# Kernel tuning notes

Hardware: AMD Instinct MI355X
Metric: run time of the kernel (lower is better)

The kernel has to match this reference:

```python
import jax, jax.numpy as jnp
import numpy as np

BN_EPS = 1e-5

def _deg_inv_sqrt(idx, n):
    deg = jax.ops.segment_sum(jnp.ones(idx.shape, jnp.float32), idx, num_segments=n)
    return jnp.where(deg > 0, 1.0 / jnp.sqrt(jnp.maximum(deg, 1.0)), 0.0)

def setup_inputs() -> dict:
    key = jax.random.key(0)
    ks = jax.random.split(key, 8)
    N, E, D, L = 50000, 500000, 128, 3
    node_ids = jax.random.randint(ks[0], (N,), 0, 343)
    src = jax.random.randint(ks[1], (E,), 0, N, dtype=jnp.int32)
    dst = jax.random.randint(ks[2], (E,), 0, N, dtype=jnp.int32)
    emb_table = jax.random.normal(ks[3], (343, D), jnp.float32)
    s = 1.0 / np.sqrt(D)
    Ws = jax.random.normal(ks[4], (L, D, D), jnp.float32) * s
    bs = jnp.zeros((L, D), jnp.float32)
    Rws = jax.random.normal(ks[5], (L, D, D), jnp.float32) * s
    Rbs = jnp.zeros((L, D), jnp.float32)
    gammas = jnp.ones((L, D), jnp.float32)
    betas = jnp.zeros((L, D), jnp.float32)
    return dict(node_ids=node_ids, src=src, dst=dst, emb_table=emb_table,
                Ws=Ws, bs=bs, Rws=Rws, Rbs=Rbs, gammas=gammas, betas=betas)

def reference(node_ids, src, dst, emb_table, Ws, bs, Rws, Rbs, gammas, betas):
    N = node_ids.shape[0]
    L = Ws.shape[0]
    # GraphConv norm='both': src side uses out-degree, dst side uses in-degree
    out_norm = _deg_inv_sqrt(src, N)  # [N]
    in_norm = _deg_inv_sqrt(dst, N)   # [N]
    x = emb_table[node_ids]           # [N, D] embedding lookup
    for l in range(L):
        # D^{-1/2} A D^{-1/2} X, then linear + bias + activation (DGL GraphConv)
        h = x * out_norm[:, None]
        agg = jax.ops.segment_sum(h[src], dst, num_segments=N) * in_norm[:, None]
        h = jax.nn.relu(agg @ Ws[l] + bs[l])
        # residual branch: activation(Linear(x)) added (dgllife GCNLayer)
        h = h + jax.nn.relu(x @ Rws[l] + Rbs[l])
        # dropout p=0 (identity), then BatchNorm1d (batch statistics)
        mu = h.mean(axis=0)
        var = h.var(axis=0)
        x = gammas[l] * (h - mu) / jnp.sqrt(var + BN_EPS) + betas[l]
    return x
```

## Files before the change

kernel.cpp:

```cpp
#include <hip/hip_runtime.h>
#include <hip/hip_bf16.h>


#define TPB 256
#define NBANK 8
#define GM 16
#define APAD 136
#define NREP 8
#define CHUNK 512
#define HSZ 12500
#define HB 32

typedef __attribute__((ext_vector_type(8))) short bf16x8;
typedef __attribute__((ext_vector_type(4))) float f32x4;

__device__ inline unsigned short f2bf(float f) {
    unsigned int u = __builtin_bit_cast(unsigned int, f);
    u += 0x7fff + ((u >> 16) & 1);
    return (unsigned short)(u >> 16);
}
__device__ inline float bf2f(unsigned short b) {
    unsigned int u = ((unsigned int)b) << 16;
    return __builtin_bit_cast(float, u);
}

__global__ void prep1(const int* __restrict__ node_ids, const float* __restrict__ emb,
                      unsigned short* __restrict__ x, int n32,
                      const float* __restrict__ Ws, const float* __restrict__ Rws,
                      unsigned short* __restrict__ Wt, unsigned short* __restrict__ Rwt,
                      int wtotal,
                      const int* __restrict__ src, const int* __restrict__ dst,
                      unsigned short* __restrict__ out_part,
                      int* __restrict__ deg_rep, int* __restrict__ rank,
                      int E, int N, int histBlocks, int degBlocks) {
    __shared__ int cnt[HSZ];
    if ((int)blockIdx.x < histBlocks) {
        int t = threadIdx.x;
        int s = blockIdx.x >> 5;
        int b = blockIdx.x & (HB - 1);
        int base = s * HSZ;
        for (int j = t; j < HSZ; j += TPB) cnt[j] = 0;
        __syncthreads();
        int per = (E + HB - 1) / HB;
        int lo = b * per;
        int hi = lo + per < E ? lo + per : E;
        for (int i = lo + t; i < hi; i += TPB) {
            int v = src[i] - base;
            if ((unsigned)v < (unsigned)HSZ) atomicAdd(&cnt[v], 1);
        }
        __syncthreads();
        for (int j = t; j < HSZ; j += TPB)
            out_part[(size_t)blockIdx.x * HSZ + j] = (unsigned short)cnt[j];
    } else if ((int)blockIdx.x < histBlocks + degBlocks) {
        int blk = blockIdx.x - histBlocks;
        int rep = blk & (NREP - 1);
        int* dd = deg_rep + (size_t)rep * N;
        int T = degBlocks * 256;
        int t0 = blk * 256 + threadIdx.x;
        int idx[4], dv[4];
        #pragma unroll
        for (int k = 0; k < 4; k++) {
            int i = t0 + k * T;
            idx[k] = (i < E) ? i : 0;
        }
        #pragma unroll
        for (int k = 0; k < 4; k++) dv[k] = dst[idx[k]];
        int r[4];
        #pragma unroll
        for (int k = 0; k < 4; k++)
            r[k] = (t0 + k * T < E) ? atomicAdd(&dd[dv[k]], 1) : 0;
        #pragma unroll
        for (int k = 0; k < 4; k++)
            if (t0 + k * T < E) rank[t0 + k * T] = r[k] | (rep << 24);
    } else {
        int gid = (blockIdx.x - histBlocks - degBlocks) * 256 + threadIdx.x;
        if (gid < n32) {
            int v = gid >> 5, c4 = gid & 31;
            int id = node_ids[v];
            float4 e = *(const float4*)&emb[id * 128 + c4 * 4];
            ushort4 o;
            o.x = f2bf(e.x); o.y = f2bf(e.y); o.z = f2bf(e.z); o.w = f2bf(e.w);
            *(ushort4*)&x[(size_t)v * 128 + c4 * 4] = o;
        }
        if (gid < wtotal) {
            int l = gid >> 14, rr = (gid >> 7) & 127, k = gid & 127;
            int sidx = l * 16384 + k * 128 + rr;
            Wt[gid]  = f2bf(Ws[sidx]);
            Rwt[gid] = f2bf(Rws[sidx]);
        }
    }
}

__global__ void scan1_norm(int* __restrict__ deg_rep,
                           const unsigned short* __restrict__ out_part,
                           float* __restrict__ out_norm, float* __restrict__ in_norm,
                           int* __restrict__ row_ptr, int* __restrict__ bsum, int n) {
    __shared__ int tmp[1024];
    int t = threadIdx.x;
    int i = blockIdx.x * 1024 + t;
    int v = 0;
    int pref[NREP];
    if (i < n) {
        int run = 0;
        #pragma unroll
        for (int r = 0; r < NREP; r++) {
            int c = deg_rep[(size_t)r * n + i];
            pref[r] = run;
            run += c;
        }
        v = run;
        int s = i / HSZ;
        int li = i - s * HSZ;
        const unsigned short* op = out_part + ((size_t)s * HB) * HSZ + li;
        int dsv = 0;
        #pragma unroll 8
        for (int r = 0; r < HB; r++) dsv += op[(size_t)r * HSZ];
        out_norm[i] = dsv > 0 ? rsqrtf((float)dsv) : 0.f;
        in_norm[i]  = v   > 0 ? rsqrtf((float)v)   : 0.f;
    }
    tmp[t] = v;
    __syncthreads();
    for (int off = 1; off < 1024; off <<= 1) {
        int add = (t >= off) ? tmp[t - off] : 0;
        __syncthreads();
        tmp[t] += add;
        __syncthreads();
    }
    int ex = tmp[t] - v;
    if (i < n) {
        row_ptr[i] = ex;
        #pragma unroll
        for (int r = 0; r < NREP; r++)
            deg_rep[(size_t)r * n + i] = pref[r] + ex;
    }
    if (t == 1023) bsum[blockIdx.x] = tmp[1023];
}

__global__ void boff_scan(const int* __restrict__ bsum, int* __restrict__ boff, int nb,
                          int2* __restrict__ col_un_pad) {
    int t = threadIdx.x;
    if (nb <= 64) {
        int orig = (t < nb) ? bsum[t] : 0;
        int v = orig;
        #pragma unroll
        for (int off = 1; off < 64; off <<= 1) {
            int u = __shfl_up(v, off);
            if (t >= off) v += u;
        }
        if (t < nb) boff[t] = v - orig;
    } else if (t == 0) {
        int run = 0;
        for (int i = 0; i < nb; i++) { boff[i] = run; run += bsum[i]; }
    }
    if (t < 8) { int2 z; z.x = 0; z.y = 0; col_un_pad[t] = z; }
}

__global__ void scatter_kernel(const int* __restrict__ src, const int* __restrict__ dst,
                               const int* __restrict__ boff,
                               const int* __restrict__ rank,
                               const float* __restrict__ out_norm,
                               const int* __restrict__ deg_rep,
                               int2* __restrict__ col_un, int E, int N, int T) {
    int t0 = blockIdx.x * blockDim.x + threadIdx.x;
    int idx[4], sv[4], dv[4], rk[4];
    #pragma unroll
    for (int k = 0; k < 4; k++) {
        int i = t0 + k * T;
        idx[k] = (i < E) ? i : 0;
    }
    #pragma unroll
    for (int k = 0; k < 4; k++) { sv[k] = src[idx[k]]; dv[k] = dst[idx[k]]; rk[k] = rank[idx[k]]; }
    int pos[4]; float nm[4];
    #pragma unroll
    for (int k = 0; k < 4; k++) {
        int rep = ((unsigned)rk[k]) >> 24;
        int lr = rk[k] & 0xFFFFFF;
        pos[k] = boff[dv[k] >> 10] + deg_rep[(size_t)rep * N + dv[k]] + lr;
        nm[k] = out_norm[sv[k]];
    }
    #pragma unroll
    for (int k = 0; k < 4; k++) {
        if (t0 + k * T < E) {
            int2 v; v.x = sv[k]; v.y = __float_as_int(nm[k]);
            col_un[pos[k]] = v;
        }
    }
}

template<bool FIRST, bool BF16OUT>
__global__ __launch_bounds__(256, 4) void fused_layer_kernel(
    const unsigned short* __restrict__ x,
    const int* __restrict__ row_ptr, const int* __restrict__ boff,
    const int2* __restrict__ col_un,
    const float* __restrict__ in_norm,
    const unsigned short* __restrict__ Wt, const unsigned short* __restrict__ Rwt,
    const float* __restrict__ bvec, const float* __restrict__ Rbvec,
    const float* __restrict__ prevStats, const float* __restrict__ prevGamma,
    const float* __restrict__ prevBeta, float nrowsf,
    float* __restrict__ nsum,
    float* __restrict__ h, unsigned short* __restrict__ hb,
    float* __restrict__ stats, int nrows, int Etot) {
    __shared__ unsigned short As[GM * APAD];
    __shared__ unsigned short Xs[GM * APAD];
    __shared__ int2 Ld[CHUNK];
    __shared__ float bsum[128], bss[128];
    __shared__ float ssc[FIRST ? 4 : 128], ssh[FIRST ? 4 : 128];
    int tid = threadIdx.x;
    int m0 = blockIdx.x * GM;
    if (tid < 128) {
        bsum[tid] = 0.f; bss[tid] = 0.f;
        if constexpr (!FIRST) {
            float s = 0.f, sq = 0.f;
            #pragma unroll
            for (int b2 = 0; b2 < NBANK; b2++) {
                s  += prevStats[b2 * 256 + tid];
                sq += prevStats[b2 * 256 + tid + 128];
            }
            float mu = s / nrowsf;
            float var = sq / nrowsf - mu * mu;
            float rstd = rsqrtf(var + 1e-5f);
            float sc = prevGamma[tid] * rstd;
            ssc[tid] = sc;
            ssh[tid] = prevBeta[tid] - sc * mu;
        }
    }
    __syncthreads();

    {
        int node = tid >> 4;
        int part = tid & 15;
        int gnode = m0 + node;
        if (gnode >= nrows) gnode = nrows - 1;
        uint4 xv = *(const uint4*)&x[(size_t)gnode * 128 + part * 8];
        if constexpr (FIRST) {
            *(uint4*)&Xs[node * APAD + part * 8] = xv;
        } else {
            const unsigned short* xs = (const unsigned short*)&xv;
            uint4 pk;
            pk.x = (unsigned int)f2bf(ssc[part * 8 + 0] * bf2f(xs[0]) + ssh[part * 8 + 0])
                 | ((unsigned int)f2bf(ssc[part * 8 + 1] * bf2f(xs[1]) + ssh[part * 8 + 1]) << 16);
            pk.y = (unsigned int)f2bf(ssc[part * 8 + 2] * bf2f(xs[2]) + ssh[part * 8 + 2])
                 | ((unsigned int)f2bf(ssc[part * 8 + 3] * bf2f(xs[3]) + ssh[part * 8 + 3]) << 16);
            pk.z = (unsigned int)f2bf(ssc[part * 8 + 4] * bf2f(xs[4]) + ssh[part * 8 + 4])
                 | ((unsigned int)f2bf(ssc[part * 8 + 5] * bf2f(xs[5]) + ssh[part * 8 + 5]) << 16);
            pk.w = (unsigned int)f2bf(ssc[part * 8 + 6] * bf2f(xs[6]) + ssh[part * 8 + 6])
                 | ((unsigned int)f2bf(ssc[part * 8 + 7] * bf2f(xs[7]) + ssh[part * 8 + 7]) << 16);
            *(uint4*)&Xs[node * APAD + part * 8] = pk;
        }
        float inv = in_norm[gnode];
        float nsumv = 0.f;
        if constexpr (!FIRST) nsumv = nsum[gnode];
        int beg = row_ptr[gnode] + boff[gnode >> 10];
        int end = (gnode == nrows - 1) ? Etot
                                       : row_ptr[gnode + 1] + boff[(gnode + 1) >> 10];
        int blkBeg = row_ptr[m0] + boff[m0 >> 10];
        int lastN = m0 + GM;
        int blkEnd = (lastN >= nrows) ? Etot : row_ptr[lastN] + boff[lastN >> 10];

        float acc[8];
        #pragma unroll
        for (int j = 0; j < 8; j++) acc[j] = 0.f;
        const unsigned short* xb = x + part * 8;

        for (int chunk = blkBeg; chunk < blkEnd; chunk += CHUNK) {
            int chunkEnd = chunk + CHUNK < blkEnd ? chunk + CHUNK : blkEnd;
            int nd = chunkEnd - chunk;
            __syncthreads();
            for (int i = tid; i < nd; i += TPB) Ld[i] = col_un[chunk + i];
            __syncthreads();
            int e0 = beg > chunk ? beg : chunk;
            int e1 = end < chunkEnd ? end : chunkEnd;
            for (int e = e0; e < e1; e += 8) {
                int rem = e1 - e;
                int base = e - chunk;
                int2 ed[8];
                #pragma unroll
                for (int j = 0; j < 8; j++)
                    ed[j] = Ld[(j < rem) ? (base + j) : base];
                uint4 q[8];
                #pragma unroll
                for (int j = 0; j < 8; j++)
                    q[j] = *(const uint4*)(xb + (size_t)(unsigned)ed[j].x * 128);
                #pragma unroll
                for (int j = 0; j < 8; j++) {
                    float nn = (j < rem) ? __int_as_float(ed[j].y) : 0.f;
                    if constexpr (FIRST) nsumv += nn;
                    const unsigned int* w = (const unsigned int*)&q[j];
                    #pragma unroll
                    for (int t = 0; t < 4; t++) {
                        acc[2 * t]     += nn * bf2f((unsigned short)w[t]);
                        acc[2 * t + 1] += nn * bf2f((unsigned short)(w[t] >> 16));
                    }
                }
            }
        }
        if constexpr (FIRST) {
            if (part == 0) nsum[gnode] = nsumv;
            #pragma unroll
            for (int j = 0; j < 8; j++) acc[j] *= inv;
        } else {
            #pragma unroll
            for (int j = 0; j < 8; j++)
                acc[j] = (ssc[part * 8 + j] * acc[j] + ssh[part * 8 + j] * nsumv) * inv;
        }
        uint4 pk;
        pk.x = (unsigned int)f2bf(acc[0]) | ((unsigned int)f2bf(acc[1]) << 16);
        pk.y = (unsigned int)f2bf(acc[2]) | ((unsigned int)f2bf(acc[3]) << 16);
        pk.z = (unsigned int)f2bf(acc[4]) | ((unsigned int)f2bf(acc[5]) << 16);
        pk.w = (unsigned int)f2bf(acc[6]) | ((unsigned int)f2bf(acc[7]) << 16);
        *(uint4*)&As[node * APAD + part * 8] = pk;
    }
    __syncthreads();

    int wave = tid >> 6;
    int lane = tid & 63;
    int m = lane & 15;
    int quad = lane >> 4;

    f32x4 accA[2], accX[2];
    #pragma unroll
    for (int t = 0; t < 2; t++) { accA[t] = (f32x4){0,0,0,0}; accX[t] = (f32x4){0,0,0,0}; }

    #pragma unroll
    for (int kc = 0; kc < 4; kc++) {
        int koff = kc * 32 + quad * 8;
        bf16x8 aA = *(const bf16x8*)&As[m * APAD + koff];
        bf16x8 aX = *(const bf16x8*)&Xs[m * APAD + koff];
        #pragma unroll
        for (int t = 0; t < 2; t++) {
            int nrow = (wave * 2 + t) * 16 + m;
            bf16x8 bW = *(const bf16x8*)&Wt[(size_t)nrow * 128 + koff];
            bf16x8 bR = *(const bf16x8*)&Rwt[(size_t)nrow * 128 + koff];
            accA[t] = __builtin_amdgcn_mfma_f32_16x16x32_bf16(aA, bW, accA[t], 0, 0, 0);
            accX[t] = __builtin_amdgcn_mfma_f32_16x16x32_bf16(aX, bR, accX[t], 0, 0, 0);
        }
    }

    #pragma unroll
    for (int t = 0; t < 2; t++) {
        int col = (wave * 2 + t) * 16 + m;
        float bW = bvec[col], bR = Rbvec[col];
        float cs = 0.f, cq = 0.f;
        #pragma unroll
        for (int reg = 0; reg < 4; reg++) {
            int gr = m0 + quad * 4 + reg;
            float hA = accA[t][reg] + bW; hA = hA > 0.f ? hA : 0.f;
            float hX = accX[t][reg] + bR; hX = hX > 0.f ? hX : 0.f;
            float v = hA + hX;
            if (gr < nrows) {
                if constexpr (BF16OUT) hb[(size_t)gr * 128 + col] = f2bf(v);
                else                   h[(size_t)gr * 128 + col] = v;
            } else {
                v = 0.f;
            }
            cs += v; cq += v * v;
        }
        cs += __shfl_xor(cs, 16); cs += __shfl_xor(cs, 32);
        cq += __shfl_xor(cq, 16); cq += __shfl_xor(cq, 32);
        if (lane < 16) {
            atomicAdd(&bsum[col], cs);
            atomicAdd(&bss[col], cq);
        }
    }
    __syncthreads();
    if (tid < 128) {
        float* sb = stats + (size_t)(blockIdx.x & (NBANK - 1)) * 256;
        atomicAdd(&sb[tid], bsum[tid]);
        atomicAdd(&sb[tid + 128], bss[tid]);
    }
}

__global__ void norm_apply_f32(const float* __restrict__ h, const float* __restrict__ stats,
                               const float* __restrict__ gamma, const float* __restrict__ beta,
                               float* __restrict__ dstp, int total4, float n) {
    __shared__ float ssc[128], ssh[128];
    int t = threadIdx.x;
    if (t < 128) {
        float s = 0.f, sq = 0.f;
        #pragma unroll
        for (int b2 = 0; b2 < NBANK; b2++) {
            s  += stats[b2 * 256 + t];
            sq += stats[b2 * 256 + t + 128];
        }
        float mu = s / n;
        float var = sq / n - mu * mu;
        float rstd = rsqrtf(var + 1e-5f);
        float sc = gamma[t] * rstd;
        ssc[t] = sc;
        ssh[t] = beta[t] - sc * mu;
    }
    __syncthreads();
    int gid = blockIdx.x * blockDim.x + t;
    if (gid >= total4) return;
    int c4 = gid & 31;
    float4 sc = *(const float4*)&ssc[c4 * 4];
    float4 sh = *(const float4*)&ssh[c4 * 4];
    float4 v = ((const float4*)h)[gid];
    float4 o;
    o.x = sc.x * v.x + sh.x;
    o.y = sc.y * v.y + sh.y;
    o.z = sc.z * v.z + sh.z;
    o.w = sc.w * v.w + sh.w;
    ((float4*)dstp)[gid] = o;
}


extern "C" void kernel_launch(void* const* d_in, const int* in_sizes, int n_in,
                              void* d_out, int out_size, void* d_ws, size_t ws_size,
                              hipStream_t stream) {
    const int*   node_ids = (const int*)d_in[0];
    const int*   src      = (const int*)d_in[1];
    const int*   dst      = (const int*)d_in[2];
    const float* emb      = (const float*)d_in[3];
    const float* Ws       = (const float*)d_in[4];
    const float* bs       = (const float*)d_in[5];
    const float* Rws      = (const float*)d_in[6];
    const float* Rbs      = (const float*)d_in[7];
    const float* gammas   = (const float*)d_in[8];
    const float* betas    = (const float*)d_in[9];

    const int N = in_sizes[0];
    const int E = in_sizes[1];
    const int D = 128;
    const int L = in_sizes[4] / (D * D);

    size_t off = 0;
    auto alloc = [&](size_t bytes) -> void* {
        void* p = (char*)d_ws + off;
        off += (bytes + 255) & ~(size_t)255;
        return p;
    };
    int NS = (N + HSZ - 1) / HSZ;
    int*   deg_rep  = (int*)alloc((size_t)NREP * N * 4);
    unsigned short* out_part = (unsigned short*)alloc((size_t)NS * HB * HSZ * 2);
    int*   rank     = (int*)alloc((size_t)E * 4);
    float* out_norm = (float*)alloc((size_t)N * 4);
    float* in_norm  = (float*)alloc((size_t)N * 4);
    float* nsum     = (float*)alloc((size_t)N * 4);
    int*   row_ptr  = (int*)alloc((size_t)(N + 1) * 4);
    int*   bsumg    = (int*)alloc(64 * 4);
    int*   boffg    = (int*)alloc(64 * 4);
    int2*  col_un   = (int2*)alloc(((size_t)E + 8) * 8);
    float* stats    = (float*)alloc((size_t)L * NBANK * 256 * 4);
    unsigned short* Wt   = (unsigned short*)alloc((size_t)L * D * D * 2);
    unsigned short* Rwt  = (unsigned short*)alloc((size_t)L * D * D * 2);
    unsigned short* x    = (unsigned short*)alloc((size_t)N * D * 2);
    unsigned short* hb0  = (unsigned short*)alloc((size_t)N * D * 2);
    unsigned short* hb1  = (unsigned short*)alloc((size_t)N * D * 2);
    float* h = (float*)d_out;

    hipMemsetAsync(deg_rep, 0, (size_t)NREP * N * 4, stream);
    hipMemsetAsync(stats, 0, (size_t)L * NBANK * 256 * 4, stream);

    int histBlocks = NS * HB;
    int degBlocks = (E + 1023) / 1024;
    int n32 = N * 32, wtotal = L * D * D;
    int embBlocks = (n32 + TPB - 1) / TPB;
    prep1<<<histBlocks + degBlocks + embBlocks, TPB, 0, stream>>>(
        node_ids, emb, x, n32, Ws, Rws, Wt, Rwt, wtotal,
        src, dst, out_part, deg_rep, rank, E, N, histBlocks, degBlocks);

    int nb = (N + 1023) / 1024;
    scan1_norm<<<nb, 1024, 0, stream>>>(deg_rep, out_part, out_norm, in_norm, row_ptr, bsumg, N);
    boff_scan<<<1, 64, 0, stream>>>(bsumg, boffg, nb, col_un + E);
    int scatBlocks = (E + 1023) / 1024;
    scatter_kernel<<<scatBlocks, TPB, 0, stream>>>(src, dst, boffg, rank, out_norm,
                                                   deg_rep, col_un, E, N, scatBlocks * 256);

    int gblocks = (N + GM - 1) / GM;
    for (int l = 0; l < L; l++) {
        const unsigned short* Wtl  = Wt  + (size_t)l * D * D;
        const unsigned short* Rwtl = Rwt + (size_t)l * D * D;
        const float* b   = bs  + (size_t)l * D;
        const float* Rb  = Rbs + (size_t)l * D;
        float* st = stats + (size_t)l * NBANK * 256;

        const unsigned short* xin = (l == 0) ? x : ((l & 1) ? hb0 : hb1);
        unsigned short* hbOut = (l < L - 1) ? (((l & 1) == 0) ? hb0 : hb1) : nullptr;
        const float* pst = (l == 0) ? nullptr : stats + (size_t)(l - 1) * NBANK * 256;
        const float* pgm = (l == 0) ? nullptr : gammas + (size_t)(l - 1) * D;
        const float* pbt = (l == 0) ? nullptr : betas  + (size_t)(l - 1) * D;

        if (l == 0) {
            fused_layer_kernel<true, true><<<gblocks, TPB, 0, stream>>>(
                xin, row_ptr, boffg, col_un, in_norm, Wtl, Rwtl, b, Rb,
                nullptr, nullptr, nullptr, (float)N, nsum, h, hbOut, st, N, E);
        } else if (l < L - 1) {
            fused_layer_kernel<false, true><<<gblocks, TPB, 0, stream>>>(
                xin, row_ptr, boffg, col_un, in_norm, Wtl, Rwtl, b, Rb,
                pst, pgm, pbt, (float)N, nsum, h, hbOut, st, N, E);
        } else {
            fused_layer_kernel<false, false><<<gblocks, TPB, 0, stream>>>(
                xin, row_ptr, boffg, col_un, in_norm, Wtl, Rwtl, b, Rb,
                pst, pgm, pbt, (float)N, nsum, h, hbOut, st, N, E);
        }
    }
    norm_apply_f32<<<(N * 32 + TPB - 1) / TPB, TPB, 0, stream>>>(
        h, stats + (size_t)(L - 1) * NBANK * 256,
        gammas + (size_t)(L - 1) * D, betas + (size_t)(L - 1) * D,
        (float*)d_out, N * 32, (float)N);
}
```

Before: 286.0 us.

## Gather first-layer features directly from embedding table via node ids in edge list

Removes the materialized bf16 embedding-lookup buffer. The scatter kernel now packs each edge's source node id (embedding row index) into the upper bits of the edge entry. The first layer then gathers fp32 rows straight from the small 343x128 table, which should stay cache-resident, instead of from an N x 128 bf16 array. This saves the write and reread of that array but doubles the bytes per gather and depends on node ids fitting in 15 bits and source indices in 17 bits.

```diff
diff --git a/kernel.cpp b/kernel.cpp
--- a/kernel.cpp
+++ b/kernel.cpp
@@ -24,9 +24,7 @@
     return __builtin_bit_cast(float, u);
 }
 
-__global__ void prep1(const int* __restrict__ node_ids, const float* __restrict__ emb,
-                      unsigned short* __restrict__ x, int n32,
-                      const float* __restrict__ Ws, const float* __restrict__ Rws,
+__global__ void prep1(const float* __restrict__ Ws, const float* __restrict__ Rws,
                       unsigned short* __restrict__ Wt, unsigned short* __restrict__ Rwt,
                       int wtotal,
                       const int* __restrict__ src, const int* __restrict__ dst,
@@ -74,14 +72,6 @@
             if (t0 + k * T < E) rank[t0 + k * T] = r[k] | (rep << 24);
     } else {
         int gid = (blockIdx.x - histBlocks - degBlocks) * 256 + threadIdx.x;
-        if (gid < n32) {
-            int v = gid >> 5, c4 = gid & 31;
-            int id = node_ids[v];
-            float4 e = *(const float4*)&emb[id * 128 + c4 * 4];
-            ushort4 o;
-            o.x = f2bf(e.x); o.y = f2bf(e.y); o.z = f2bf(e.z); o.w = f2bf(e.w);
-            *(ushort4*)&x[(size_t)v * 128 + c4 * 4] = o;
-        }
         if (gid < wtotal) {
             int l = gid >> 14, rr = (gid >> 7) & 127, k = gid & 127;
             int sidx = l * 16384 + k * 128 + rr;
@@ -159,6 +149,7 @@
                                const int* __restrict__ boff,
                                const int* __restrict__ rank,
                                const float* __restrict__ out_norm,
+                               const int* __restrict__ node_ids,
                                const int* __restrict__ deg_rep,
                                int2* __restrict__ col_un, int E, int N, int T) {
     int t0 = blockIdx.x * blockDim.x + threadIdx.x;
@@ -170,18 +161,19 @@
     }
     #pragma unroll
     for (int k = 0; k < 4; k++) { sv[k] = src[idx[k]]; dv[k] = dst[idx[k]]; rk[k] = rank[idx[k]]; }
-    int pos[4]; float nm[4];
+    int pos[4]; float nm[4]; int nid[4];
     #pragma unroll
     for (int k = 0; k < 4; k++) {
         int rep = ((unsigned)rk[k]) >> 24;
         int lr = rk[k] & 0xFFFFFF;
         pos[k] = boff[dv[k] >> 10] + deg_rep[(size_t)rep * N + dv[k]] + lr;
         nm[k] = out_norm[sv[k]];
+        nid[k] = node_ids[sv[k]];
     }
     #pragma unroll
     for (int k = 0; k < 4; k++) {
         if (t0 + k * T < E) {
-            int2 v; v.x = sv[k]; v.y = __float_as_int(nm[k]);
+            int2 v; v.x = sv[k] | (nid[k] << 17); v.y = __float_as_int(nm[k]);
             col_un[pos[k]] = v;
         }
     }
@@ -190,6 +182,7 @@
 template<bool FIRST, bool BF16OUT>
 __global__ __launch_bounds__(256, 4) void fused_layer_kernel(
     const unsigned short* __restrict__ x,
+    const int* __restrict__ node_ids, const float* __restrict__ emb,
     const int* __restrict__ row_ptr, const int* __restrict__ boff,
     const int2* __restrict__ col_un,
     const float* __restrict__ in_norm,
@@ -231,10 +224,19 @@
         int part = tid & 15;
         int gnode = m0 + node;
         if (gnode >= nrows) gnode = nrows - 1;
-        uint4 xv = *(const uint4*)&x[(size_t)gnode * 128 + part * 8];
         if constexpr (FIRST) {
-            *(uint4*)&Xs[node * APAD + part * 8] = xv;
+            int id0 = node_ids[gnode];
+            const float* er = emb + (size_t)id0 * 128 + part * 8;
+            float4 e0 = *(const float4*)er;
+            float4 e1 = *(const float4*)(er + 4);
+            uint4 pk;
+            pk.x = (unsigned int)f2bf(e0.x) | ((unsigned int)f2bf(e0.y) << 16);
+            pk.y = (unsigned int)f2bf(e0.z) | ((unsigned int)f2bf(e0.w) << 16);
+            pk.z = (unsigned int)f2bf(e1.x) | ((unsigned int)f2bf(e1.y) << 16);
+            pk.w = (unsigned int)f2bf(e1.z) | ((unsigned int)f2bf(e1.w) << 16);
+            *(uint4*)&Xs[node * APAD + part * 8] = pk;
         } else {
+            uint4 xv = *(const uint4*)&x[(size_t)gnode * 128 + part * 8];
             const unsigned short* xs = (const unsigned short*)&xv;
             uint4 pk;
             pk.x = (unsigned int)f2bf(ssc[part * 8 + 0] * bf2f(xs[0]) + ssh[part * 8 + 0])
@@ -261,6 +263,7 @@
         #pragma unroll
         for (int j = 0; j < 8; j++) acc[j] = 0.f;
         const unsigned short* xb = x + part * 8;
+        const float* eb = emb + part * 8;
 
         for (int chunk = blkBeg; chunk < blkEnd; chunk += CHUNK) {
             int chunkEnd = chunk + CHUNK < blkEnd ? chunk + CHUNK : blkEnd;
@@ -277,19 +280,46 @@
                 #pragma unroll
                 for (int j = 0; j < 8; j++)
                     ed[j] = Ld[(j < rem) ? (base + j) : base];
-                uint4 q[8];
-                #pragma unroll
-                for (int j = 0; j < 8; j++)
-                    q[j] = *(const uint4*)(xb + (size_t)(unsigned)ed[j].x * 128);
-                #pragma unroll
-                for (int j = 0; j < 8; j++) {
-                    float nn = (j < rem) ? __int_as_float(ed[j].y) : 0.f;
-                    if constexpr (FIRST) nsumv += nn;
-                    const unsigned int* w = (const unsigned int*)&q[j];
+                if constexpr (FIRST) {
+                    float4 q0[8];
                     #pragma unroll
-                    for (int t = 0; t < 4; t++) {
-                        acc[2 * t]     += nn * bf2f((unsigned short)w[t]);
-                        acc[2 * t + 1] += nn * bf2f((unsigned short)(w[t] >> 16));
+                    for (int j = 0; j < 8; j++) {
+                        unsigned id = ((unsigned)ed[j].x) >> 17;
+                        q0[j] = *(const float4*)(eb + (size_t)id * 128);
+                    }
+                    float nn[8];
+                    #pragma unroll
+                    for (int j = 0; j < 8; j++) {
+                        nn[j] = (j < rem) ? __int_as_float(ed[j].y) : 0.f;
+                        nsumv += nn[j];
+                        acc[0] += nn[j] * q0[j].x; acc[1] += nn[j] * q0[j].y;
+                        acc[2] += nn[j] * q0[j].z; acc[3] += nn[j] * q0[j].w;
+                    }
+                    float4 q1[8];
+                    #pragma unroll
+                    for (int j = 0; j < 8; j++) {
+                        unsigned id = ((unsigned)ed[j].x) >> 17;
+                        q1[j] = *(const float4*)(eb + (size_t)id * 128 + 4);
+                    }
+                    #pragma unroll
+                    for (int j = 0; j < 8; j++) {
+                        acc[4] += nn[j] * q1[j].x; acc[5] += nn[j] * q1[j].y;
+                        acc[6] += nn[j] * q1[j].z; acc[7] += nn[j] * q1[j].w;
+                    }
+                } else {
+                    uint4 q[8];
+                    #pragma unroll
+                    for (int j = 0; j < 8; j++)
+                        q[j] = *(const uint4*)(xb + (size_t)(((unsigned)ed[j].x) & 0x1FFFFu) * 128);
+                    #pragma unroll
+                    for (int j = 0; j < 8; j++) {
+                        float nn = (j < rem) ? __int_as_float(ed[j].y) : 0.f;
+                        const unsigned int* w = (const unsigned int*)&q[j];
+                        #pragma unroll
+                        for (int t = 0; t < 4; t++) {
+                            acc[2 * t]     += nn * bf2f((unsigned short)w[t]);
+                            acc[2 * t + 1] += nn * bf2f((unsigned short)(w[t] >> 16));
+                        }
                     }
                 }
             }
@@ -444,7 +474,6 @@
     float* stats    = (float*)alloc((size_t)L * NBANK * 256 * 4);
     unsigned short* Wt   = (unsigned short*)alloc((size_t)L * D * D * 2);
     unsigned short* Rwt  = (unsigned short*)alloc((size_t)L * D * D * 2);
-    unsigned short* x    = (unsigned short*)alloc((size_t)N * D * 2);
     unsigned short* hb0  = (unsigned short*)alloc((size_t)N * D * 2);
     unsigned short* hb1  = (unsigned short*)alloc((size_t)N * D * 2);
     float* h = (float*)d_out;
@@ -454,10 +483,10 @@
 
     int histBlocks = NS * HB;
     int degBlocks = (E + 1023) / 1024;
-    int n32 = N * 32, wtotal = L * D * D;
-    int embBlocks = (n32 + TPB - 1) / TPB;
-    prep1<<<histBlocks + degBlocks + embBlocks, TPB, 0, stream>>>(
-        node_ids, emb, x, n32, Ws, Rws, Wt, Rwt, wtotal,
+    int wtotal = L * D * D;
+    int wBlocks = (wtotal + TPB - 1) / TPB;
+    prep1<<<histBlocks + degBlocks + wBlocks, TPB, 0, stream>>>(
+        Ws, Rws, Wt, Rwt, wtotal,
         src, dst, out_part, deg_rep, rank, E, N, histBlocks, degBlocks);
 
     int nb = (N + 1023) / 1024;
@@ -465,7 +494,8 @@
     boff_scan<<<1, 64, 0, stream>>>(bsumg, boffg, nb, col_un + E);
     int scatBlocks = (E + 1023) / 1024;
     scatter_kernel<<<scatBlocks, TPB, 0, stream>>>(src, dst, boffg, rank, out_norm,
-                                                   deg_rep, col_un, E, N, scatBlocks * 256);
+                                                   node_ids, deg_rep, col_un, E, N,
+                                                   scatBlocks * 256);
 
     int gblocks = (N + GM - 1) / GM;
     for (int l = 0; l < L; l++) {
@@ -475,7 +505,7 @@
         const float* Rb  = Rbs + (size_t)l * D;
         float* st = stats + (size_t)l * NBANK * 256;
 
-        const unsigned short* xin = (l == 0) ? x : ((l & 1) ? hb0 : hb1);
+        const unsigned short* xin = (l == 0) ? nullptr : ((l & 1) ? hb0 : hb1);
         unsigned short* hbOut = (l < L - 1) ? (((l & 1) == 0) ? hb0 : hb1) : nullptr;
         const float* pst = (l == 0) ? nullptr : stats + (size_t)(l - 1) * NBANK * 256;
         const float* pgm = (l == 0) ? nullptr : gammas + (size_t)(l - 1) * D;
@@ -483,15 +513,15 @@
 
         if (l == 0) {
             fused_layer_kernel<true, true><<<gblocks, TPB, 0, stream>>>(
-                xin, row_ptr, boffg, col_un, in_norm, Wtl, Rwtl, b, Rb,
+                nullptr, node_ids, emb, row_ptr, boffg, col_un, in_norm, Wtl, Rwtl, b, Rb,
                 nullptr, nullptr, nullptr, (float)N, nsum, h, hbOut, st, N, E);
         } else if (l < L - 1) {
             fused_layer_kernel<false, true><<<gblocks, TPB, 0, stream>>>(
-                xin, row_ptr, boffg, col_un, in_norm, Wtl, Rwtl, b, Rb,
+                xin, nullptr, nullptr, row_ptr, boffg, col_un, in_norm, Wtl, Rwtl, b, Rb,
                 pst, pgm, pbt, (float)N, nsum, h, hbOut, st, N, E);
         } else {
             fused_layer_kernel<false, false><<<gblocks, TPB, 0, stream>>>(
-                xin, row_ptr, boffg, col_un, in_norm, Wtl, Rwtl, b, Rb,
+                xin, nullptr, nullptr, row_ptr, boffg, col_un, in_norm, Wtl, Rwtl, b, Rb,
                 pst, pgm, pbt, (float)N, nsum, h, hbOut, st, N, E);
         }
     }
```

After: 289.7 us. No clear change (+1.3%).
